# Optimization experiments

Hardware: AMD Instinct MI355X
Metric: run time of the kernel (lower is better)

## Reference

```python
import jax, jax.numpy as jnp
import numpy as np

N_NODES = 100000
N_EDGES = 1600000
IN_C, HID_C, OUT_C = 128, 128, 64


def setup_inputs() -> dict:
    key = jax.random.key(0)
    ks = jax.random.split(key, 8)
    x = jax.random.normal(ks[0], (N_NODES, IN_C), dtype=jnp.float32)
    edge_index = jax.random.randint(ks[1], (2, N_EDGES), 0, N_NODES, dtype=jnp.int64)
    # SAGEConv params: lin_l (aggregated neighbors, with bias), lin_r (root, no bias)
    s1 = 1.0 / np.sqrt(IN_C)
    s2 = 1.0 / np.sqrt(HID_C)
    W1_l = jax.random.uniform(ks[2], (IN_C, HID_C), jnp.float32, -s1, s1)
    b1_l = jnp.zeros((HID_C,), jnp.float32)
    W1_r = jax.random.uniform(ks[3], (IN_C, HID_C), jnp.float32, -s1, s1)
    W2_l = jax.random.uniform(ks[4], (HID_C, OUT_C), jnp.float32, -s2, s2)
    b2_l = jnp.zeros((OUT_C,), jnp.float32)
    W2_r = jax.random.uniform(ks[5], (HID_C, OUT_C), jnp.float32, -s2, s2)
    return {"x": x, "edge_index": edge_index, "W1_l": W1_l, "b1_l": b1_l,
            "W1_r": W1_r, "W2_l": W2_l, "b2_l": b2_l, "W2_r": W2_r}


def _sage_conv(x, src, dst, W_l, b_l, W_r):
    # gather source features, scatter-max reduce onto destinations
    msg = x[src]                                             # [E, C]
    aggr = jax.ops.segment_max(msg, dst, num_segments=N_NODES)
    aggr = jnp.where(jnp.isfinite(aggr), aggr, 0.0)          # isolated nodes -> 0 (PyG behavior)
    return aggr @ W_l + b_l + x @ W_r


def reference(x, edge_index, W1_l, b1_l, W1_r, W2_l, b2_l, W2_r):
    src, dst = edge_index[0], edge_index[1]
    h = _sage_conv(x, src, dst, W1_l, b1_l, W1_r)
    h = jax.nn.relu(h)
    # dropout is identity in eval mode
    out = _sage_conv(h, src, dst, W2_l, b2_l, W2_r)
    return out
```

## Files before the change

kernel.cpp:

```cpp
#include <hip/hip_runtime.h>
#include <cstdint>

#define NNODES 100000
#define NEDGES 1600000
#define NBKT   196
#define CAP    9216
#define BIN_CHUNK 4096
#define GBIN ((NEDGES + BIN_CHUNK - 1) / BIN_CHUNK)
#define GCVT (NNODES * 128 / 8 / 256)

typedef __attribute__((ext_vector_type(8))) __bf16 bf16x8;
typedef __attribute__((ext_vector_type(4))) float f32x4;
typedef short v2s __attribute__((ext_vector_type(2)));

__device__ __forceinline__ unsigned short f2bf_rne(float f) {
    unsigned int u = __float_as_uint(f);
    u += 0x7fffu + ((u >> 16) & 1u);
    return (unsigned short)(u >> 16);
}
__device__ __forceinline__ unsigned encdec(unsigned u) {
    return u ^ (((u & 0x80008000u) >> 15) * 0x7FFFu);
}
__device__ __forceinline__ unsigned pkmax(unsigned a, unsigned b) {
    v2s r = __builtin_elementwise_max(__builtin_bit_cast(v2s, a), __builtin_bit_cast(v2s, b));
    return __builtin_bit_cast(unsigned, r);
}
__device__ __forceinline__ uint4 pkmax4(uint4 a, uint4 b) {
    uint4 r;
    r.x = pkmax(a.x, b.x); r.y = pkmax(a.y, b.y);
    r.z = pkmax(a.z, b.z); r.w = pkmax(a.w, b.w);
    return r;
}


__global__ __launch_bounds__(256) void prep1_kernel(
        const float* __restrict__ W1l, const float* __restrict__ W1r,
        const float* __restrict__ W2l, const float* __restrict__ W2r,
        uint4* __restrict__ Wf1, uint4* __restrict__ Wf2,
        int* __restrict__ bucketFill) {
    if (blockIdx.x == 24) { bucketFill[threadIdx.x] = 0; return; }
    int t = blockIdx.x * 256 + threadIdx.x;
    unsigned short s[8];
    if (t < 4096) {
        int h = t >> 11, kt = (t >> 9) & 3, nt = (t >> 6) & 7, lane = t & 63;
        const float* W = h ? W1r : W1l;
        int k0 = kt * 32 + (lane >> 4) * 8;
        int col = nt * 16 + (lane & 15);
#pragma unroll
        for (int j = 0; j < 8; ++j) s[j] = f2bf_rne(W[(k0 + j) * 128 + col]);
        uint4 o;
        o.x = (unsigned)s[0] | ((unsigned)s[1] << 16);
        o.y = (unsigned)s[2] | ((unsigned)s[3] << 16);
        o.z = (unsigned)s[4] | ((unsigned)s[5] << 16);
        o.w = (unsigned)s[6] | ((unsigned)s[7] << 16);
        Wf1[t] = o;
    } else {
        int u = t - 4096;
        int h = u >> 10, kt = (u >> 8) & 3, nt = (u >> 6) & 3, lane = u & 63;
        const float* W = h ? W2r : W2l;
        int k0 = kt * 32 + (lane >> 4) * 8;
        int col = nt * 16 + (lane & 15);
#pragma unroll
        for (int j = 0; j < 8; ++j) s[j] = f2bf_rne(W[(k0 + j) * 64 + col]);
        uint4 o;
        o.x = (unsigned)s[0] | ((unsigned)s[1] << 16);
        o.y = (unsigned)s[2] | ((unsigned)s[3] << 16);
        o.z = (unsigned)s[4] | ((unsigned)s[5] << 16);
        o.w = (unsigned)s[6] | ((unsigned)s[7] << 16);
        Wf2[u] = o;
    }
}

__global__ __launch_bounds__(256) void prep2_kernel(
        const int* __restrict__ src, const int* __restrict__ dst,
        unsigned int* __restrict__ binArr, int* __restrict__ bucketFill,
        const float4* __restrict__ xin, uint4* __restrict__ xeout, int nE) {
    if (blockIdx.x >= GBIN) {
        int t = (blockIdx.x - GBIN) * 256 + threadIdx.x;
        int s = t / (NNODES * 2);
        int rem = t - s * (NNODES * 2);
        int n = rem >> 1, hh = rem & 1;
        int f = n * 32 + s * 4 + hh * 2;
        float4 v0 = xin[f], v1 = xin[f + 1];
        uint4 o;
        o.x = encdec((unsigned)f2bf_rne(v0.x) | ((unsigned)f2bf_rne(v0.y) << 16));
        o.y = encdec((unsigned)f2bf_rne(v0.z) | ((unsigned)f2bf_rne(v0.w) << 16));
        o.z = encdec((unsigned)f2bf_rne(v1.x) | ((unsigned)f2bf_rne(v1.y) << 16));
        o.w = encdec((unsigned)f2bf_rne(v1.z) | ((unsigned)f2bf_rne(v1.w) << 16));
        xeout[t] = o;
        return;
    }
    __shared__ unsigned int stage[BIN_CHUNK];
    __shared__ unsigned char bof[BIN_CHUNK];
    __shared__ int cnt[256], cstart[256], cfill[256], gbase[256];
    const int tid = threadIdx.x;
    const int blockStart = blockIdx.x * BIN_CHUNK;
    const int chunkN = min(BIN_CHUNK, nE - blockStart);
    cnt[tid] = 0;
    __syncthreads();
    int myd[16], mys[16];
#pragma unroll
    for (int i = 0; i < 16; ++i) {
        int idx = i * 256 + tid;
        if (idx < chunkN) {
            myd[i] = dst[blockStart + idx];
            mys[i] = src[blockStart + idx];
            atomicAdd(&cnt[myd[i] >> 9], 1);
        }
    }
    __syncthreads();
    int v = cnt[tid];
    for (int off = 1; off < 256; off <<= 1) {
        int add = (tid >= off) ? cnt[tid - off] : 0;
        __syncthreads();
        cnt[tid] += add;
        __syncthreads();
    }
    cstart[tid] = cnt[tid] - v;
    cfill[tid] = cnt[tid] - v;
    if (tid < NBKT && v > 0) gbase[tid] = atomicAdd(&bucketFill[tid], v);
    __syncthreads();
#pragma unroll
    for (int i = 0; i < 16; ++i) {
        int idx = i * 256 + tid;
        if (idx < chunkN) {
            int b = myd[i] >> 9;
            int p = atomicAdd(&cfill[b], 1);
            stage[p] = ((unsigned)(myd[i] & 511) << 17) | (unsigned)mys[i];
            bof[p] = (unsigned char)b;
        }
    }
    __syncthreads();
#pragma unroll
    for (int i = 0; i < 16; ++i) {
        int idx = i * 256 + tid;
        if (idx < chunkN) {
            int b = bof[idx];
            int slot = gbase[b] + (idx - cstart[b]);
            if (slot < CAP) binArr[(size_t)b * CAP + slot] = stage[idx];
        }
    }
}

__global__ __launch_bounds__(512) void build_csr_kernel(
        const unsigned int* __restrict__ binArr, const int* __restrict__ bucketFill,
        unsigned int* __restrict__ sortedSrc,
        int* __restrict__ rowBeg, int* __restrict__ rowEnd) {
    __shared__ unsigned int stage[CAP];
    __shared__ int ncnt[512], nstart[512];
    const int b = blockIdx.x;
    const int t = threadIdx.x;
    const int cnt_b = min(bucketFill[b], CAP);
    ncnt[t] = 0;
    __syncthreads();
    for (int i = t; i < cnt_b; i += 512) {
        unsigned int e = binArr[(size_t)b * CAP + i];
        stage[i] = e;
        atomicAdd(&ncnt[e >> 17], 1);
    }
    __syncthreads();
    int v = ncnt[t];
    for (int off = 1; off < 512; off <<= 1) {
        int add = (t >= off) ? ncnt[t - off] : 0;
        __syncthreads();
        ncnt[t] += add;
        __syncthreads();
    }
    int start = ncnt[t] - v;
    nstart[t] = start;
    int n = (b << 9) + t;
    if (n < NNODES) {
        rowBeg[n] = b * CAP + start;
        rowEnd[n] = b * CAP + start + v;
    }
    __syncthreads();
    for (int i = t; i < cnt_b; i += 512) {
        unsigned int e = stage[i];
        int p = atomicAdd(&nstart[e >> 17], 1);
        sortedSrc[(size_t)b * CAP + p] = e & 0x1FFFFu;
    }
}

__global__ __launch_bounds__(256) void aggregate_sl(
        const uint4* __restrict__ xsl,
        const int* __restrict__ rowBeg,
        const int* __restrict__ rowEnd,
        const unsigned int* __restrict__ sortedSrc,
        uint4* __restrict__ asl,
        int nN) {
    const int s    = blockIdx.x & 7;
    const int g    = blockIdx.x >> 3;
    const int wv   = threadIdx.x >> 6;
    const int lane = threadIdx.x & 63;
    const int k    = lane >> 3;
    const int sub  = (lane >> 1) & 3;
    const int h    = lane & 1;
    const int n    = g * 32 + wv * 8 + k;
    const size_t sbase = (size_t)s * nN;

    const int beg = rowBeg[n], end = rowEnd[n];
    const int m = end - beg;

    int maxm = m;
    maxm = max(maxm, __shfl_xor(maxm, 8));
    maxm = max(maxm, __shfl_xor(maxm, 16));
    maxm = max(maxm, __shfl_xor(maxm, 32));

    int id0 = 0, id1 = 0, id2 = 0, id3 = 0;
    if (m > 0) {
        id0 = (int)sortedSrc[min(beg + sub,      end - 1)];
        id1 = (int)sortedSrc[min(beg + 4 + sub,  end - 1)];
        id2 = (int)sortedSrc[min(beg + 8 + sub,  end - 1)];
        id3 = (int)sortedSrc[min(beg + 12 + sub, end - 1)];
    }
    uint4 p0 = xsl[(sbase + id0) * 2 + h];
    uint4 p1 = xsl[(sbase + id1) * 2 + h];
    uint4 p2 = xsl[(sbase + id2) * 2 + h];
    uint4 p3 = xsl[(sbase + id3) * 2 + h];
    uint4 acc = pkmax4(pkmax4(p0, p1), pkmax4(p2, p3));

    for (int e0 = 16; e0 < maxm; e0 += 4) {
        int idt = (m > 0) ? (int)sortedSrc[min(beg + e0 + sub, end - 1)] : 0;
        uint4 q = xsl[(sbase + idt) * 2 + h];
        acc = pkmax4(acc, q);
    }

    acc.x = pkmax(acc.x, (unsigned)__shfl_xor((int)acc.x, 2));
    acc.y = pkmax(acc.y, (unsigned)__shfl_xor((int)acc.y, 2));
    acc.z = pkmax(acc.z, (unsigned)__shfl_xor((int)acc.z, 2));
    acc.w = pkmax(acc.w, (unsigned)__shfl_xor((int)acc.w, 2));
    acc.x = pkmax(acc.x, (unsigned)__shfl_xor((int)acc.x, 4));
    acc.y = pkmax(acc.y, (unsigned)__shfl_xor((int)acc.y, 4));
    acc.z = pkmax(acc.z, (unsigned)__shfl_xor((int)acc.z, 4));
    acc.w = pkmax(acc.w, (unsigned)__shfl_xor((int)acc.w, 4));

    const unsigned ok = (m > 0) ? 0xFFFFFFFFu : 0u;
    if (sub == 0) {
        uint4 o;
        o.x = acc.x & ok; o.y = acc.y & ok; o.z = acc.z & ok; o.w = acc.w & ok;
        asl[(sbase + n) * 2 + h] = o;
    }
}

template<int BN, bool RELU, bool ENCOUT, typename OutT>
__global__ __launch_bounds__(256, 4) void sage_gemm_lean(
        const uint4* __restrict__ AggE,
        const uint4* __restrict__ RootE,
        const uint4* __restrict__ Wf,
        const float* __restrict__ bias,
        OutT* __restrict__ C,
        int M) {
    constexpr int NT = BN / 16;
    const int tid = threadIdx.x;
    const int w = tid >> 6;
    const int lane = tid & 63;
    const int quad = lane >> 4;
    const int mrow = lane & 15;
    const int base0 = blockIdx.x * 128 + w * 32;

    const int r0 = min(base0 + mrow, M - 1);
    const int r1 = min(base0 + 16 + mrow, M - 1);

    f32x4 acc[2][NT];
#pragma unroll
    for (int mt = 0; mt < 2; ++mt)
#pragma unroll
        for (int nt = 0; nt < NT; ++nt) acc[mt][nt] = (f32x4){0.f, 0.f, 0.f, 0.f};

#pragma unroll
    for (int kt = 0; kt < 4; ++kt) {
        const int q = kt * 4 + quad;
        const size_t sl = ((size_t)(q >> 1) * M) * 2 + (q & 1);
        uint4 ta0 = AggE[sl + (size_t)r0 * 2];
        uint4 ta1 = AggE[sl + (size_t)r1 * 2];
        uint4 tr0 = RootE[sl + (size_t)r0 * 2];
        uint4 tr1 = RootE[sl + (size_t)r1 * 2];
        ta0.x = encdec(ta0.x); ta0.y = encdec(ta0.y); ta0.z = encdec(ta0.z); ta0.w = encdec(ta0.w);
        ta1.x = encdec(ta1.x); ta1.y = encdec(ta1.y); ta1.z = encdec(ta1.z); ta1.w = encdec(ta1.w);
        tr0.x = encdec(tr0.x); tr0.y = encdec(tr0.y); tr0.z = encdec(tr0.z); tr0.w = encdec(tr0.w);
        tr1.x = encdec(tr1.x); tr1.y = encdec(tr1.y); tr1.z = encdec(tr1.z); tr1.w = encdec(tr1.w);
        bf16x8 aa0 = __builtin_bit_cast(bf16x8, ta0);
        bf16x8 aa1 = __builtin_bit_cast(bf16x8, ta1);
        bf16x8 ar0 = __builtin_bit_cast(bf16x8, tr0);
        bf16x8 ar1 = __builtin_bit_cast(bf16x8, tr1);
#pragma unroll
        for (int nt = 0; nt < NT; ++nt) {
            bf16x8 b0 = __builtin_bit_cast(bf16x8, Wf[(kt * NT + nt) * 64 + lane]);
            acc[0][nt] = __builtin_amdgcn_mfma_f32_16x16x32_bf16(aa0, b0, acc[0][nt], 0, 0, 0);
            acc[1][nt] = __builtin_amdgcn_mfma_f32_16x16x32_bf16(aa1, b0, acc[1][nt], 0, 0, 0);
            bf16x8 b1 = __builtin_bit_cast(bf16x8, Wf[((4 + kt) * NT + nt) * 64 + lane]);
            acc[0][nt] = __builtin_amdgcn_mfma_f32_16x16x32_bf16(ar0, b1, acc[0][nt], 0, 0, 0);
            acc[1][nt] = __builtin_amdgcn_mfma_f32_16x16x32_bf16(ar1, b1, acc[1][nt], 0, 0, 0);
        }
    }

#pragma unroll
    for (int mt = 0; mt < 2; ++mt) {
        const int rowD = base0 + mt * 16 + quad * 4;
#pragma unroll
        for (int nt = 0; nt < NT; ++nt) {
            int col = nt * 16 + mrow;
            float bv = bias[col];
#pragma unroll
            for (int r = 0; r < 4; ++r) {
                int grow = rowD + r;
                if (grow < M) {
                    float v = acc[mt][nt][r] + bv;
                    if (RELU) v = fmaxf(v, 0.0f);
                    if constexpr (ENCOUT) {
                        unsigned u = f2bf_rne(v);
                        u ^= ((u >> 15) & 1u) * 0x7FFFu;
                        C[((size_t)nt * M + grow) * 16 + mrow] = (OutT)u;
                    } else {
                        C[(size_t)grow * BN + col] = (OutT)v;
                    }
                }
            }
        }
    }
}

extern "C" void kernel_launch(void* const* d_in, const int* in_sizes, int n_in,
                              void* d_out, int out_size, void* d_ws, size_t ws_size,
                              hipStream_t stream) {
    const float* x   = (const float*)d_in[0];
    const int*   ei  = (const int*)d_in[1];
    const float* W1l = (const float*)d_in[2];
    const float* b1l = (const float*)d_in[3];
    const float* W1r = (const float*)d_in[4];
    const float* W2l = (const float*)d_in[5];
    const float* b2l = (const float*)d_in[6];
    const float* W2r = (const float*)d_in[7];
    float* out = (float*)d_out;

    const int* src = ei;
    const int* dst = ei + NEDGES;

    char* ws = (char*)d_ws;
    unsigned short* xe    = (unsigned short*)ws; ws += (size_t)NNODES * 128 * 2;
    unsigned short* he    = (unsigned short*)ws; ws += (size_t)NNODES * 128 * 2;
    unsigned short* aggrE = (unsigned short*)ws; ws += (size_t)NNODES * 128 * 2;
    unsigned int* binArr    = (unsigned int*)ws; ws += (size_t)NBKT * CAP * 4;
    unsigned int* sortedSrc = (unsigned int*)ws; ws += (size_t)NBKT * CAP * 4;
    int* rowBeg     = (int*)ws; ws += (size_t)NNODES * 4;
    int* rowEnd     = (int*)ws; ws += (size_t)NNODES * 4;
    int* bucketFill = (int*)ws; ws += 256 * 4;
    uint4* Wf1 = (uint4*)ws; ws += 4096 * 16;
    uint4* Wf2 = (uint4*)ws; ws += 2048 * 16;

    const int gAgg = (NNODES / 32) * 8;
    const int gGemm = (NNODES + 127) / 128;

    prep1_kernel<<<25, 256, 0, stream>>>(W1l, W1r, W2l, W2r, Wf1, Wf2, bucketFill);
    prep2_kernel<<<GBIN + GCVT, 256, 0, stream>>>(src, dst, binArr, bucketFill,
                                                  (const float4*)x, (uint4*)xe, NEDGES);
    build_csr_kernel<<<NBKT, 512, 0, stream>>>(binArr, bucketFill, sortedSrc, rowBeg, rowEnd);

    aggregate_sl<<<gAgg, 256, 0, stream>>>((const uint4*)xe, rowBeg, rowEnd, sortedSrc,
                                           (uint4*)aggrE, NNODES);
    sage_gemm_lean<128, true, true, unsigned short><<<gGemm, 256, 0, stream>>>(
        (const uint4*)aggrE, (const uint4*)xe, Wf1, b1l, he, NNODES);
    aggregate_sl<<<gAgg, 256, 0, stream>>>((const uint4*)he, rowBeg, rowEnd, sortedSrc,
                                           (uint4*)aggrE, NNODES);
    sage_gemm_lean<64, false, false, float><<<gGemm, 256, 0, stream>>>(
        (const uint4*)aggrE, (const uint4*)he, Wf2, b2l, out, NNODES);
}
```

Measured before the change: 322.3 us.

## Widen feature slabs to 64 channels and gather one neighbor per 8-lane group

Changes the bf16 feature layout from eight 16-channel slabs to two 64-channel slabs, so each node row in a slab is 128 contiguous bytes. Aggregation now has 8 lanes cooperatively load one neighbor's 64 channels, broadcasts neighbor ids by shuffle, and processes 8 neighbors per iteration with no cross-lane reduction. The aim is fewer, more coalesced gather transactions per edge. The cost is more shuffles and padded iterations for nodes with low degree, plus matching index changes in the conversion and GEMM kernels.

```diff
diff --git a/kernel.cpp b/kernel.cpp
--- a/kernel.cpp
+++ b/kernel.cpp
@@ -7,7 +7,7 @@
 #define CAP    9216
 #define BIN_CHUNK 4096
 #define GBIN ((NEDGES + BIN_CHUNK - 1) / BIN_CHUNK)
-#define GCVT (NNODES * 128 / 8 / 256)
+#define GCVT (NNODES * 16 / 256)
 
 typedef __attribute__((ext_vector_type(8))) __bf16 bf16x8;
 typedef __attribute__((ext_vector_type(4))) float f32x4;
@@ -77,10 +77,10 @@
         const float4* __restrict__ xin, uint4* __restrict__ xeout, int nE) {
     if (blockIdx.x >= GBIN) {
         int t = (blockIdx.x - GBIN) * 256 + threadIdx.x;
-        int s = t / (NNODES * 2);
-        int rem = t - s * (NNODES * 2);
-        int n = rem >> 1, hh = rem & 1;
-        int f = n * 32 + s * 4 + hh * 2;
+        int s = t / (NNODES * 8);
+        int rem = t - s * (NNODES * 8);
+        int n = rem >> 3, j = rem & 7;
+        int f = n * 32 + s * 16 + j * 2;
         float4 v0 = xin[f], v1 = xin[f + 1];
         uint4 o;
         o.x = encdec((unsigned)f2bf_rne(v0.x) | ((unsigned)f2bf_rne(v0.y) << 16));
@@ -181,22 +181,25 @@
     }
 }
 
-__global__ __launch_bounds__(256) void aggregate_sl(
+__global__ __launch_bounds__(256) void aggregate_sl2(
         const uint4* __restrict__ xsl,
         const int* __restrict__ rowBeg,
         const int* __restrict__ rowEnd,
         const unsigned int* __restrict__ sortedSrc,
         uint4* __restrict__ asl,
         int nN) {
-    const int s    = blockIdx.x & 7;
-    const int g    = blockIdx.x >> 3;
+    const int r    = blockIdx.x & 7;
+    const int c    = blockIdx.x >> 3;
+    const int s    = r >> 2;
+    const int g    = c * 4 + (r & 3);
+    if (g * 32 >= nN) return;
     const int wv   = threadIdx.x >> 6;
     const int lane = threadIdx.x & 63;
     const int k    = lane >> 3;
-    const int sub  = (lane >> 1) & 3;
-    const int h    = lane & 1;
+    const int j    = lane & 7;
+    const int kb   = k << 3;
     const int n    = g * 32 + wv * 8 + k;
-    const size_t sbase = (size_t)s * nN;
+    const size_t srow = (size_t)s * nN;
 
     const int beg = rowBeg[n], end = rowEnd[n];
     const int m = end - beg;
@@ -206,40 +209,44 @@
     maxm = max(maxm, __shfl_xor(maxm, 16));
     maxm = max(maxm, __shfl_xor(maxm, 32));
 
-    int id0 = 0, id1 = 0, id2 = 0, id3 = 0;
-    if (m > 0) {
-        id0 = (int)sortedSrc[min(beg + sub,      end - 1)];
-        id1 = (int)sortedSrc[min(beg + 4 + sub,  end - 1)];
-        id2 = (int)sortedSrc[min(beg + 8 + sub,  end - 1)];
-        id3 = (int)sortedSrc[min(beg + 12 + sub, end - 1)];
-    }
-    uint4 p0 = xsl[(sbase + id0) * 2 + h];
-    uint4 p1 = xsl[(sbase + id1) * 2 + h];
-    uint4 p2 = xsl[(sbase + id2) * 2 + h];
-    uint4 p3 = xsl[(sbase + id3) * 2 + h];
-    uint4 acc = pkmax4(pkmax4(p0, p1), pkmax4(p2, p3));
-
-    for (int e0 = 16; e0 < maxm; e0 += 4) {
-        int idt = (m > 0) ? (int)sortedSrc[min(beg + e0 + sub, end - 1)] : 0;
-        uint4 q = xsl[(sbase + idt) * 2 + h];
-        acc = pkmax4(acc, q);
-    }
-
-    acc.x = pkmax(acc.x, (unsigned)__shfl_xor((int)acc.x, 2));
-    acc.y = pkmax(acc.y, (unsigned)__shfl_xor((int)acc.y, 2));
-    acc.z = pkmax(acc.z, (unsigned)__shfl_xor((int)acc.z, 2));
-    acc.w = pkmax(acc.w, (unsigned)__shfl_xor((int)acc.w, 2));
-    acc.x = pkmax(acc.x, (unsigned)__shfl_xor((int)acc.x, 4));
-    acc.y = pkmax(acc.y, (unsigned)__shfl_xor((int)acc.y, 4));
-    acc.z = pkmax(acc.z, (unsigned)__shfl_xor((int)acc.z, 4));
-    acc.w = pkmax(acc.w, (unsigned)__shfl_xor((int)acc.w, 4));
-
-    const unsigned ok = (m > 0) ? 0xFFFFFFFFu : 0u;
-    if (sub == 0) {
-        uint4 o;
-        o.x = acc.x & ok; o.y = acc.y & ok; o.z = acc.z & ok; o.w = acc.w & ok;
-        asl[(sbase + n) * 2 + h] = o;
-    }
+    int idv = (m > 0) ? (int)sortedSrc[min(beg + j, end - 1)] : 0;
+    int s0 = __shfl(idv, kb | 0), s1 = __shfl(idv, kb | 1);
+    int s2 = __shfl(idv, kb | 2), s3 = __shfl(idv, kb | 3);
+    int s4 = __shfl(idv, kb | 4), s5 = __shfl(idv, kb | 5);
+    int s6 = __shfl(idv, kb | 6), s7 = __shfl(idv, kb | 7);
+    uint4 q0 = xsl[(srow + s0) * 8 + j];
+    uint4 q1 = xsl[(srow + s1) * 8 + j];
+    uint4 q2 = xsl[(srow + s2) * 8 + j];
+    uint4 q3 = xsl[(srow + s3) * 8 + j];
+    uint4 q4 = xsl[(srow + s4) * 8 + j];
+    uint4 q5 = xsl[(srow + s5) * 8 + j];
+    uint4 q6 = xsl[(srow + s6) * 8 + j];
+    uint4 q7 = xsl[(srow + s7) * 8 + j];
+    uint4 acc = pkmax4(pkmax4(pkmax4(q0, q1), pkmax4(q2, q3)),
+                       pkmax4(pkmax4(q4, q5), pkmax4(q6, q7)));
+
+    for (int e0 = 8; e0 < maxm; e0 += 8) {
+        idv = (m > 0) ? (int)sortedSrc[min(beg + e0 + j, end - 1)] : 0;
+        s0 = __shfl(idv, kb | 0); s1 = __shfl(idv, kb | 1);
+        s2 = __shfl(idv, kb | 2); s3 = __shfl(idv, kb | 3);
+        s4 = __shfl(idv, kb | 4); s5 = __shfl(idv, kb | 5);
+        s6 = __shfl(idv, kb | 6); s7 = __shfl(idv, kb | 7);
+        q0 = xsl[(srow + s0) * 8 + j];
+        q1 = xsl[(srow + s1) * 8 + j];
+        q2 = xsl[(srow + s2) * 8 + j];
+        q3 = xsl[(srow + s3) * 8 + j];
+        q4 = xsl[(srow + s4) * 8 + j];
+        q5 = xsl[(srow + s5) * 8 + j];
+        q6 = xsl[(srow + s6) * 8 + j];
+        q7 = xsl[(srow + s7) * 8 + j];
+        acc = pkmax4(acc, pkmax4(pkmax4(pkmax4(q0, q1), pkmax4(q2, q3)),
+                                 pkmax4(pkmax4(q4, q5), pkmax4(q6, q7))));
+    }
+
+    uint4 o;
+    if (m > 0) { o = acc; }
+    else       { o.x = o.y = o.z = o.w = 0u; }
+    asl[(srow + n) * 8 + j] = o;
 }
 
 template<int BN, bool RELU, bool ENCOUT, typename OutT>
@@ -270,11 +277,12 @@
 #pragma unroll
     for (int kt = 0; kt < 4; ++kt) {
         const int q = kt * 4 + quad;
-        const size_t sl = ((size_t)(q >> 1) * M) * 2 + (q & 1);
-        uint4 ta0 = AggE[sl + (size_t)r0 * 2];
-        uint4 ta1 = AggE[sl + (size_t)r1 * 2];
-        uint4 tr0 = RootE[sl + (size_t)r0 * 2];
-        uint4 tr1 = RootE[sl + (size_t)r1 * 2];
+        const size_t sl = (size_t)(q >> 3) * M;
+        const int jj = q & 7;
+        uint4 ta0 = AggE[(sl + r0) * 8 + jj];
+        uint4 ta1 = AggE[(sl + r1) * 8 + jj];
+        uint4 tr0 = RootE[(sl + r0) * 8 + jj];
+        uint4 tr1 = RootE[(sl + r1) * 8 + jj];
         ta0.x = encdec(ta0.x); ta0.y = encdec(ta0.y); ta0.z = encdec(ta0.z); ta0.w = encdec(ta0.w);
         ta1.x = encdec(ta1.x); ta1.y = encdec(ta1.y); ta1.z = encdec(ta1.z); ta1.w = encdec(ta1.w);
         tr0.x = encdec(tr0.x); tr0.y = encdec(tr0.y); tr0.z = encdec(tr0.z); tr0.w = encdec(tr0.w);
@@ -310,7 +318,7 @@
                     if constexpr (ENCOUT) {
                         unsigned u = f2bf_rne(v);
                         u ^= ((u >> 15) & 1u) * 0x7FFFu;
-                        C[((size_t)nt * M + grow) * 16 + mrow] = (OutT)u;
+                        C[((size_t)(col >> 6) * M + grow) * 64 + (col & 63)] = (OutT)u;
                     } else {
                         C[(size_t)grow * BN + col] = (OutT)v;
                     }
@@ -348,7 +356,7 @@
     uint4* Wf1 = (uint4*)ws; ws += 4096 * 16;
     uint4* Wf2 = (uint4*)ws; ws += 2048 * 16;
 
-    const int gAgg = (NNODES / 32) * 8;
+    const int gAgg = 8 * ((NNODES / 32 + 3) / 4);
     const int gGemm = (NNODES + 127) / 128;
 
     prep1_kernel<<<25, 256, 0, stream>>>(W1l, W1r, W2l, W2r, Wf1, Wf2, bucketFill);
@@ -356,12 +364,12 @@
                                                   (const float4*)x, (uint4*)xe, NEDGES);
     build_csr_kernel<<<NBKT, 512, 0, stream>>>(binArr, bucketFill, sortedSrc, rowBeg, rowEnd);
 
-    aggregate_sl<<<gAgg, 256, 0, stream>>>((const uint4*)xe, rowBeg, rowEnd, sortedSrc,
-                                           (uint4*)aggrE, NNODES);
+    aggregate_sl2<<<gAgg, 256, 0, stream>>>((const uint4*)xe, rowBeg, rowEnd, sortedSrc,
+                                            (uint4*)aggrE, NNODES);
     sage_gemm_lean<128, true, true, unsigned short><<<gGemm, 256, 0, stream>>>(
         (const uint4*)aggrE, (const uint4*)xe, Wf1, b1l, he, NNODES);
-    aggregate_sl<<<gAgg, 256, 0, stream>>>((const uint4*)he, rowBeg, rowEnd, sortedSrc,
-                                           (uint4*)aggrE, NNODES);
+    aggregate_sl2<<<gAgg, 256, 0, stream>>>((const uint4*)he, rowBeg, rowEnd, sortedSrc,
+                                            (uint4*)aggrE, NNODES);
     sage_gemm_lean<64, false, false, float><<<gGemm, 256, 0, stream>>>(
         (const uint4*)aggrE, (const uint4*)he, Wf2, b2l, out, NNODES);
 }
```

Result: faster. 283.7 us (-12.0%).
